# Performance work log

Hardware: AMD Instinct MI355X
Metric: run time of the kernel (lower is better)

The kernel has to match this reference:

```python
import jax, jax.numpy as jnp
import numpy as np

DIM = 1024
DIM_FEAT = 384
HIDDEN = 1024
HEADS = 16
D_HEAD = HIDDEN // HEADS
SCALE = D_HEAD ** -0.5
EPS = 1e-5


def _layernorm(x, g, b):
    mu = jnp.mean(x, axis=-1, keepdims=True)
    var = jnp.var(x, axis=-1, keepdims=True)
    return (x - mu) * jax.lax.rsqrt(var + EPS) * g + b


def _split_heads(t):
    b, n, _ = t.shape
    return t.reshape(b, n, HEADS, D_HEAD).transpose(0, 2, 1, 3)  # b h n d


def _merge_heads(t):
    b, h, n, d = t.shape
    return t.transpose(0, 2, 1, 3).reshape(b, n, h * d)


def _attn(q, k, v):
    dots = jnp.einsum('bhnd,bhmd->bhnm', q, k) * SCALE
    attn = jax.nn.softmax(dots, axis=-1)
    return jnp.einsum('bhnm,bhmd->bhnd', attn, v)


def setup_inputs() -> dict:
    key = jax.random.key(0)
    ks = jax.random.split(key, 10)
    B, N = 2, 2048
    s = lambda fan: 1.0 / np.sqrt(fan)
    return {
        'x': jax.random.normal(ks[0], (B, N, DIM), jnp.float32),
        'feature': jax.random.normal(ks[1], (B, N, DIM_FEAT), jnp.float32),
        'norm_g': jnp.ones((DIM,), jnp.float32),
        'norm_b': jnp.zeros((DIM,), jnp.float32),
        'W_cq': jax.random.normal(ks[2], (DIM, HIDDEN), jnp.float32) * s(DIM),
        'W_ckv': jax.random.normal(ks[3], (DIM_FEAT, 2 * HIDDEN), jnp.float32) * s(DIM_FEAT),
        'W_sqkv': jax.random.normal(ks[4], (DIM, 3 * HIDDEN), jnp.float32) * s(DIM),
        'ffn_g': jnp.ones((DIM,), jnp.float32),
        'ffn_b': jnp.zeros((DIM,), jnp.float32),
        'W1': jax.random.normal(ks[5], (DIM, 4 * DIM), jnp.float32) * s(DIM),
        'b1': jnp.zeros((4 * DIM,), jnp.float32),
        'W2': jax.random.normal(ks[6], (4 * DIM, DIM), jnp.float32) * s(4 * DIM),
        'b2': jnp.zeros((DIM,), jnp.float32),
    }


def reference(x, feature, norm_g, norm_b, W_cq, W_ckv, W_sqkv, ffn_g, ffn_b, W1, b1, W2, b2):
    # cross attention
    xn = _layernorm(x, norm_g, norm_b)
    q = _split_heads(xn @ W_cq)
    kv = feature @ W_ckv
    k, v = jnp.split(kv, 2, axis=-1)
    cross = _merge_heads(_attn(q, _split_heads(k), _split_heads(v))) + x
    # self attention (shared norm)
    cn = _layernorm(cross, norm_g, norm_b)
    qkv = cn @ W_sqkv
    sq, sk, sv = (_split_heads(t) for t in jnp.split(qkv, 3, axis=-1))
    self_tok = _merge_heads(_attn(sq, sk, sv)) + cross
    # FFN with its own layernorm
    h = _layernorm(self_tok, ffn_g, ffn_b)
    h = jax.nn.gelu(h @ W1 + b1, approximate=False)
    out = h @ W2 + b2
    return out + self_tok
```

## Files before the change

kernel.cpp:

```cpp
#include <hip/hip_runtime.h>
#include <math.h>
#include <stdint.h>

typedef __attribute__((ext_vector_type(8)))  short   short8;
typedef __attribute__((ext_vector_type(4)))  short   short4v;
typedef __attribute__((ext_vector_type(8)))  __bf16  bf16x8;
typedef __attribute__((ext_vector_type(4)))  float   f32x4;
typedef __attribute__((ext_vector_type(16))) float   f32x16;

__device__ __forceinline__ unsigned short f2b(float f) {
    union { float f; unsigned u; } v; v.f = f;
    unsigned r = v.u + 0x7FFF + ((v.u >> 16) & 1);
    return (unsigned short)(r >> 16);
}

__device__ __forceinline__ f32x4 mfma_bf16(bf16x8 a, bf16x8 b, f32x4 c) {
    return __builtin_amdgcn_mfma_f32_16x16x32_bf16(a, b, c, 0, 0, 0);
}

__device__ __forceinline__ f32x16 mfma32(bf16x8 a, bf16x8 b, f32x16 c) {
    return __builtin_amdgcn_mfma_f32_32x32x16_bf16(a, b, c, 0, 0, 0);
}

__device__ __forceinline__ unsigned cvt_pk_bf16(float lo, float hi) {
    unsigned r;
    asm volatile("v_cvt_pk_bf16_f32 %0, %1, %2" : "=v"(r) : "v"(lo), "v"(hi));
    return r;
}

__device__ __forceinline__ void gload_lds16(const unsigned short* g, unsigned short* l) {
    __builtin_amdgcn_global_load_lds(
        (const __attribute__((address_space(1))) void*)g,
        (__attribute__((address_space(3))) void*)l,
        16, 0, 0);
}

template <int N>
__device__ __forceinline__ void wait_vmcnt() {
    if constexpr (N == 0)       asm volatile("s_waitcnt vmcnt(0)" ::: "memory");
    else if constexpr (N == 4)  asm volatile("s_waitcnt vmcnt(4)" ::: "memory");
    else if constexpr (N == 6)  asm volatile("s_waitcnt vmcnt(6)" ::: "memory");
    else if constexpr (N == 8)  asm volatile("s_waitcnt vmcnt(8)" ::: "memory");
    else                        static_assert(N == 0 || N == 4 || N == 6 || N == 8, "add vmcnt case");
}

#define QSCALE 0.18033688011112042592f

__global__ __launch_bounds__(256) void wconv_t(const float* __restrict__ W,
                                               unsigned short* __restrict__ Wt,
                                               int K, int N) {
    __shared__ float tile[32][33];
    int bk = blockIdx.x * 32;
    int bn = blockIdx.y * 32;
    int tx = threadIdx.x & 31, ty = threadIdx.x >> 5;
#pragma unroll
    for (int i = 0; i < 4; ++i) {
        int r = ty + i * 8;
        tile[r][tx] = W[(size_t)(bk + r) * N + bn + tx];
    }
    __syncthreads();
#pragma unroll
    for (int i = 0; i < 4; ++i) {
        int r = ty + i * 8;
        Wt[(size_t)(bn + r) * K + bk + tx] = f2b(tile[tx][r]);
    }
}

__global__ __launch_bounds__(256) void fconv(const float* __restrict__ in,
                                             unsigned short* __restrict__ out, int n4) {
    int i = blockIdx.x * 256 + threadIdx.x;
    if (i >= n4) return;
    f32x4 v = ((const f32x4*)in)[i];
    short4v o;
    o.x = (short)f2b(v.x); o.y = (short)f2b(v.y);
    o.z = (short)f2b(v.z); o.w = (short)f2b(v.w);
    ((short4v*)out)[i] = o;
}

__global__ __launch_bounds__(256) void lnorm(const float* __restrict__ x,
                                             const float* __restrict__ g,
                                             const float* __restrict__ bta,
                                             unsigned short* __restrict__ out) {
    int row = blockIdx.x;
    const f32x4* xr = (const f32x4*)(x + (size_t)row * 1024);
    int t = threadIdx.x;
    f32x4 v = xr[t];
    float s  = v.x + v.y + v.z + v.w;
    float s2 = v.x * v.x + v.y * v.y + v.z * v.z + v.w * v.w;
#pragma unroll
    for (int m = 1; m < 64; m <<= 1) {
        s  += __shfl_xor(s, m);
        s2 += __shfl_xor(s2, m);
    }
    __shared__ float rs[8];
    int w = t >> 6;
    if ((t & 63) == 0) { rs[w] = s; rs[4 + w] = s2; }
    __syncthreads();
    s  = rs[0] + rs[1] + rs[2] + rs[3];
    s2 = rs[4] + rs[5] + rs[6] + rs[7];
    float mean = s * (1.0f / 1024.0f);
    float var  = s2 * (1.0f / 1024.0f) - mean * mean;
    float rstd = rsqrtf(var + 1e-5f);
    f32x4 gv = ((const f32x4*)g)[t];
    f32x4 bv = ((const f32x4*)bta)[t];
    short4v o;
    o.x = (short)f2b((v.x - mean) * rstd * gv.x + bv.x);
    o.y = (short)f2b((v.y - mean) * rstd * gv.y + bv.y);
    o.z = (short)f2b((v.z - mean) * rstd * gv.z + bv.z);
    o.w = (short)f2b((v.w - mean) * rstd * gv.w + bv.w);
    ((short4v*)(out + (size_t)row * 1024))[t] = o;
}

template <int WM, int WN, int MI, int NI, int EPI, bool SCQ>
__global__ __launch_bounds__(WM * WN * 64, 2)
void gemm8(const unsigned short* __restrict__ A,
           const unsigned short* __restrict__ Bt,
           void* __restrict__ C,
           const float* __restrict__ bias,
           const float* __restrict__ resid,
           int M, int N, int K, int scale_cols) {
    constexpr int BM = WM * MI * 16;
    constexpr int BN = WN * NI * 16;
    constexpr int THREADS = WM * WN * 64;
    constexpr int ROWS = THREADS / 8;
    constexpr int IA = BM / ROWS;
    constexpr int IB = BN / ROWS;

    const int nwg = gridDim.x;
    const int nby = N / BN;
    int flat = blockIdx.x;
    int wk = (flat & 7) * (nwg >> 3) + (flat >> 3);
    const int m0 = (wk / nby) * BM;
    const int n0 = (wk % nby) * BN;

    __shared__ unsigned short As[2][BM * 64];
    __shared__ unsigned short Bs[2][BN * 64];

    const int tid  = threadIdx.x;
    const int lane = tid & 63;
    const int wid  = tid >> 6;
    const int wm = wid / WN, wn = wid % WN;
    const int l15 = lane & 15, q4 = lane >> 4, xw = lane & 7;

    const int sr = tid >> 3;
    const int sg = (tid & 7) ^ (sr & 7);

    const unsigned short* ag = A  + (size_t)(m0 + sr) * K + sg * 8;
    const unsigned short* bg = Bt + (size_t)(n0 + sr) * K + sg * 8;

    f32x4 acc[MI][NI] = {};

    auto STAGE = [&](int d, int t) {
        const int k0 = t * 64;
#pragma unroll
        for (int i = 0; i < IA; ++i)
            gload_lds16(ag + (size_t)(i * ROWS) * K + k0, &As[d][i * ROWS * 64 + tid * 8]);
#pragma unroll
        for (int i = 0; i < IB; ++i)
            gload_lds16(bg + (size_t)(i * ROWS) * K + k0, &Bs[d][i * ROWS * 64 + tid * 8]);
    };

    const int NT = K >> 6;
    STAGE(0, 0);

    for (int t = 0; t < NT; ++t) {
        const int c = t & 1;
        if (t + 1 < NT) STAGE(c ^ 1, t + 1);
        __builtin_amdgcn_sched_barrier(0);
        if (t + 1 < NT) wait_vmcnt<IA + IB>();
        else            wait_vmcnt<0>();
        __builtin_amdgcn_s_barrier();
        __builtin_amdgcn_sched_barrier(0);
#pragma unroll
        for (int h = 0; h < 2; ++h) {
            bf16x8 a[MI], b[NI];
            const int gsl = h * 4 + q4;
#pragma unroll
            for (int mi = 0; mi < MI; ++mi)
                a[mi] = *(const bf16x8*)&As[c][(wm * MI * 16 + mi * 16 + l15) * 64 + ((gsl ^ xw) << 3)];
#pragma unroll
            for (int ni = 0; ni < NI; ++ni)
                b[ni] = *(const bf16x8*)&Bs[c][(wn * NI * 16 + ni * 16 + l15) * 64 + ((gsl ^ xw) << 3)];
            __builtin_amdgcn_s_setprio(1);
#pragma unroll
            for (int mi = 0; mi < MI; ++mi)
#pragma unroll
                for (int ni = 0; ni < NI; ++ni)
                    acc[mi][ni] = mfma_bf16(a[mi], b[ni], acc[mi][ni]);
            __builtin_amdgcn_s_setprio(0);
        }
        __builtin_amdgcn_sched_barrier(0);
        __builtin_amdgcn_s_barrier();
    }

    const int rb = m0 + wm * MI * 16 + q4 * 4;
    const int cb = n0 + wn * NI * 16 + l15;
    float bv[NI];
    if (EPI >= 1) {
#pragma unroll
        for (int ni = 0; ni < NI; ++ni) bv[ni] = bias[cb + ni * 16];
    }
#pragma unroll
    for (int mi = 0; mi < MI; ++mi) {
#pragma unroll
        for (int r = 0; r < 4; ++r) {
            const int row = rb + mi * 16 + r;
#pragma unroll
            for (int ni = 0; ni < NI; ++ni) {
                const int col = cb + ni * 16;
                float v = acc[mi][ni][r];
                if (EPI == 0) {
                    if (SCQ && col < scale_cols) v *= QSCALE;
                    ((unsigned short*)C)[(size_t)row * N + col] = f2b(v);
                } else if (EPI == 1) {
                    v += bv[ni];
                    v = 0.5f * v * (1.0f + erff(v * 0.70710678118f));
                    ((unsigned short*)C)[(size_t)row * N + col] = f2b(v);
                } else {
                    v += bv[ni] + resid[(size_t)row * N + col];
                    ((float*)C)[(size_t)row * N + col] = v;
                }
            }
        }
    }
}

template <int EPI, bool SCQ>
__global__ __launch_bounds__(512, 2)
void gemm256(const unsigned short* __restrict__ A,
             const unsigned short* __restrict__ Bt,
             void* __restrict__ C,
             const float* __restrict__ bias,
             const float* __restrict__ resid,
             int M, int N, int K, int scale_cols) {
    const int nby = N / 256;
    const int nwg = gridDim.x;
    int flat = blockIdx.x;
    int wk = (flat & 7) * (nwg >> 3) + (flat >> 3);
    const int m0 = (wk / nby) * 256;
    const int n0 = (wk % nby) * 256;

    __shared__ unsigned short As[2][256 * 64];
    __shared__ unsigned short Bs[2][256 * 64];

    const int tid  = threadIdx.x;
    const int lane = tid & 63;
    const int wid  = tid >> 6;
    const int wm = wid >> 2, wn = wid & 3;
    const int l15 = lane & 15, q4 = lane >> 4, xw = lane & 7;

    const int sr = tid >> 3;
    const int sg = (tid & 7) ^ (sr & 7);

    const unsigned short* ag = A  + (size_t)(m0 + sr) * K + sg * 8;
    const unsigned short* bg = Bt + (size_t)(n0 + sr) * K + sg * 8;

    f32x4 acc[8][4] = {};

#define SA256(d, t, i) gload_lds16(ag + (size_t)((i) * 64) * K + (t) * 64, &As[d][(i) * 4096 + tid * 8])
#define SB256(d, t, i) gload_lds16(bg + (size_t)((i) * 64) * K + (t) * 64, &Bs[d][(i) * 4096 + tid * 8])

    const int NT = K >> 6;
#pragma unroll
    for (int i = 0; i < 4; ++i) { SA256(0, 0, i); SB256(0, 0, i); }
    wait_vmcnt<0>();
    __builtin_amdgcn_s_barrier();

    for (int t = 0; t < NT; ++t) {
        const int c = t & 1;
        const bool pf = (t + 1 < NT);
        bf16x8 breg[4];
#pragma unroll
        for (int p = 0; p < 4; ++p) {
            const int h = p >> 1, mh = p & 1;
            const int col = ((h * 4 + q4) ^ xw) << 3;
            if ((p & 1) == 0) {
#pragma unroll
                for (int ni = 0; ni < 4; ++ni)
                    breg[ni] = *(const bf16x8*)&Bs[c][(wn * 64 + ni * 16 + l15) * 64 + col];
            }
            bf16x8 a[4];
#pragma unroll
            for (int mi = 0; mi < 4; ++mi)
                a[mi] = *(const bf16x8*)&As[c][(wm * 128 + mh * 64 + mi * 16 + l15) * 64 + col];
            if (pf) {
                if (p == 0)      { SA256(c ^ 1, t + 1, 0); SB256(c ^ 1, t + 1, 0); SA256(c ^ 1, t + 1, 1); }
                else if (p == 1) { SB256(c ^ 1, t + 1, 1); SA256(c ^ 1, t + 1, 2); SB256(c ^ 1, t + 1, 2); }
                else if (p == 2) { SA256(c ^ 1, t + 1, 3); SB256(c ^ 1, t + 1, 3); }
            }
            __builtin_amdgcn_sched_barrier(0);
            asm volatile("s_waitcnt lgkmcnt(0)" ::: "memory");
            __builtin_amdgcn_sched_barrier(0);
            __builtin_amdgcn_s_setprio(1);
#pragma unroll
            for (int mi = 0; mi < 4; ++mi)
#pragma unroll
                for (int ni = 0; ni < 4; ++ni)
                    acc[mh * 4 + mi][ni] = mfma_bf16(a[mi], breg[ni], acc[mh * 4 + mi][ni]);
            __builtin_amdgcn_s_setprio(0);
            __builtin_amdgcn_sched_barrier(0);
            if (p == 3) wait_vmcnt<0>();
            __builtin_amdgcn_s_barrier();
        }
    }
#undef SA256
#undef SB256

    const int rb = m0 + wm * 128 + q4 * 4;
    const int cb = n0 + wn * 64 + l15;
    float bv[4];
    if (EPI >= 1) {
#pragma unroll
        for (int ni = 0; ni < 4; ++ni) bv[ni] = bias[cb + ni * 16];
    }
#pragma unroll
    for (int ai = 0; ai < 8; ++ai) {
#pragma unroll
        for (int r = 0; r < 4; ++r) {
            const int row = rb + ai * 16 + r;
#pragma unroll
            for (int ni = 0; ni < 4; ++ni) {
                const int col = cb + ni * 16;
                float v = acc[ai][ni][r];
                if (EPI == 0) {
                    if (SCQ && col < scale_cols) v *= QSCALE;
                    ((unsigned short*)C)[(size_t)row * N + col] = f2b(v);
                } else if (EPI == 1) {
                    v += bv[ni];
                    v = 0.5f * v * (1.0f + erff(v * 0.70710678118f));
                    ((unsigned short*)C)[(size_t)row * N + col] = f2b(v);
                } else {
                    v += bv[ni] + resid[(size_t)row * N + col];
                    ((float*)C)[(size_t)row * N + col] = v;
                }
            }
        }
    }
}

__global__ __launch_bounds__(256) void kvpack(const unsigned short* __restrict__ src,
                                              int stride, int k_off, int v_off,
                                              unsigned short* __restrict__ pack) {
    const int oct = blockIdx.x;
    const int bh  = blockIdx.y;
    const int b = bh >> 4, h = bh & 15;
    const int tid = threadIdx.x;
    const int lane = tid & 63;
    const int sl = tid >> 6;
    const int l31 = lane & 31, l5 = lane >> 5;
    __shared__ unsigned short Kl[32 * 64], Vl[32 * 64];
    const int r = tid >> 3, c8 = (tid & 7) * 8;
    for (int t8 = 0; t8 < 8; ++t8) {
        const int kt = oct * 8 + t8;
        const int kb = kt * 32;
        *(short8*)&Kl[r * 64 + c8] = *(const short8*)&src[(size_t)(b * 2048 + kb + r) * stride + k_off + h * 64 + c8];
        *(short8*)&Vl[r * 64 + c8] = *(const short8*)&src[(size_t)(b * 2048 + kb + r) * stride + v_off + h * 64 + c8];
        __syncthreads();
        unsigned short* o = pack + (size_t)bh * 262144 + (size_t)kt * 4096;
        *(short8*)&o[sl * 512 + lane * 8] = *(const short8*)&Kl[l31 * 64 + sl * 16 + l5 * 8];
        {
            const int dh = sl >> 1, c2 = sl & 1;
            short8 vv;
#pragma unroll
            for (int j = 0; j < 8; ++j)
                vv[j] = (short)Vl[(c2 * 16 + l5 * 8 + j) * 64 + dh * 32 + l31];
            *(short8*)&o[(4 + sl) * 512 + lane * 8] = vv;
        }
        __syncthreads();
    }
}

__global__ __launch_bounds__(128) void attn(const unsigned short* __restrict__ Q, int q_stride, int q_off,
                                            const unsigned short* __restrict__ pack,
                                            const float* __restrict__ res,
                                            float* __restrict__ out) {
    const int bid = blockIdx.x;
    const int slot = bid >> 3;
    const int bh = (bid & 7) * 4 + (slot >> 5);
    const int qt = slot & 31;
    const int b = bh >> 4, h = bh & 15;
    const int lane = threadIdx.x & 63, w = threadIdx.x >> 6;
    const int l31 = lane & 31, l5 = lane >> 5;

    __shared__ unsigned short lds[2][8192];

    const int q0 = qt * 64 + w * 32;

    const unsigned short* qp = Q + (size_t)(b * 2048 + q0 + l31) * q_stride + q_off + h * 64 + l5 * 8;
    bf16x8 qf[4];
#pragma unroll
    for (int i = 0; i < 4; ++i) qf[i] = *(const bf16x8*)&qp[i * 16];

    const unsigned short* pkb = pack + (size_t)bh * 262144;

    f32x16 oacc[2] = {};
    f32x16 lacc = {};

    auto STAGE = [&](int d, int t) {
        const unsigned short* s = pkb + (size_t)t * 8192;
#pragma unroll
        for (int i = 0; i < 8; ++i) {
            const int ch = i * 2 + w;
            gload_lds16(s + ch * 512 + lane * 8, &lds[d][ch * 512 + lane * 8]);
        }
    };

    STAGE(0, 0);

    for (int t = 0; t < 32; ++t) {
        const int cur = t & 1;
        if (t + 1 < 32) STAGE(cur ^ 1, t + 1);
        __builtin_amdgcn_sched_barrier(0);
        if (t + 1 < 32) wait_vmcnt<8>();
        else            wait_vmcnt<0>();
        __builtin_amdgcn_s_barrier();
        __builtin_amdgcn_sched_barrier(0);

        const unsigned short* L = &lds[cur][lane * 8];

        bf16x8 kf[2][4];
#pragma unroll
        for (int ks = 0; ks < 2; ++ks)
#pragma unroll
            for (int i = 0; i < 4; ++i)
                kf[ks][i] = *(const bf16x8*)&L[ks * 4096 + i * 512];

        f32x16 s0 = {}, s1 = {};
        __builtin_amdgcn_s_setprio(1);
#pragma unroll
        for (int i = 0; i < 4; ++i) s0 = mfma32(kf[0][i], qf[i], s0);
#pragma unroll
        for (int i = 0; i < 4; ++i) s1 = mfma32(kf[1][i], qf[i], s1);
        __builtin_amdgcn_s_setprio(0);

        bf16x8 vf[2][4];
#pragma unroll
        for (int dh = 0; dh < 2; ++dh)
#pragma unroll
            for (int jj = 0; jj < 4; ++jj)
                vf[dh][jj] = *(const bf16x8*)&L[(jj >> 1) * 4096 + (4 + dh * 2 + (jj & 1)) * 512];

        float p0[16], p1[16];
#pragma unroll
        for (int r = 0; r < 16; ++r) p0[r] = __builtin_amdgcn_exp2f(s0[r]);
#pragma unroll
        for (int r = 0; r < 16; ++r) p1[r] = __builtin_amdgcn_exp2f(s1[r]);
#pragma unroll
        for (int r = 0; r < 16; ++r) lacc[r] += p0[r] + p1[r];

        bf16x8 pf[4];
#pragma unroll
        for (int half = 0; half < 2; ++half) {
            const float* p = half ? p1 : p0;
#pragma unroll
            for (int c = 0; c < 2; ++c) {
                unsigned a0 = cvt_pk_bf16(p[8 * c + 0], p[8 * c + 1]);
                unsigned a1 = cvt_pk_bf16(p[8 * c + 4], p[8 * c + 5]);
                unsigned b0 = cvt_pk_bf16(p[8 * c + 2], p[8 * c + 3]);
                unsigned b1 = cvt_pk_bf16(p[8 * c + 6], p[8 * c + 7]);
                asm volatile("v_permlane32_swap_b32 %0, %1" : "+v"(a0), "+v"(a1));
                asm volatile("v_permlane32_swap_b32 %0, %1" : "+v"(b0), "+v"(b1));
                union { unsigned u[4]; bf16x8 v; } pu;
                pu.u[0] = a0; pu.u[1] = b0; pu.u[2] = a1; pu.u[3] = b1;
                pf[half * 2 + c] = pu.v;
            }
        }

        __builtin_amdgcn_s_setprio(1);
#pragma unroll
        for (int dh = 0; dh < 2; ++dh)
#pragma unroll
            for (int jj = 0; jj < 4; ++jj)
                oacc[dh] = mfma32(vf[dh][jj], pf[jj], oacc[dh]);
        __builtin_amdgcn_s_setprio(0);

        __builtin_amdgcn_s_barrier();
    }

    float lsum[16];
#pragma unroll
    for (int r = 0; r < 16; ++r) lsum[r] = lacc[r];
#pragma unroll
    for (int off = 8; off >= 1; off >>= 1)
#pragma unroll
        for (int r = 0; r < off; ++r) lsum[r] += lsum[r + off];
    const float l = lsum[0] + __shfl_xor(lsum[0], 32);

    const float inv = 1.0f / l;
    const size_t rowoff = (size_t)(b * 2048 + q0 + l31) * 1024 + h * 64;
#pragma unroll
    for (int dh = 0; dh < 2; ++dh) {
#pragma unroll
        for (int g = 0; g < 4; ++g) {
            const int col = dh * 32 + g * 8 + l5 * 4;
            f32x4 rv = *(const f32x4*)&res[rowoff + col];
            f32x4 ov;
#pragma unroll
            for (int r = 0; r < 4; ++r) ov[r] = oacc[dh][g * 4 + r] * inv + rv[r];
            *(f32x4*)&out[rowoff + col] = ov;
        }
    }
}

extern "C" void kernel_launch(void* const* d_in, const int* in_sizes, int n_in,
                              void* d_out, int out_size, void* d_ws, size_t ws_size,
                              hipStream_t stream) {
    const float* x      = (const float*)d_in[0];
    const float* feat   = (const float*)d_in[1];
    const float* norm_g = (const float*)d_in[2];
    const float* norm_b = (const float*)d_in[3];
    const float* W_cq   = (const float*)d_in[4];
    const float* W_ckv  = (const float*)d_in[5];
    const float* W_sqkv = (const float*)d_in[6];
    const float* ffn_g  = (const float*)d_in[7];
    const float* ffn_b  = (const float*)d_in[8];
    const float* W1     = (const float*)d_in[9];
    const float* b1     = (const float*)d_in[10];
    const float* W2     = (const float*)d_in[11];
    const float* b2     = (const float*)d_in[12];
    float* out = (float*)d_out;

    char* ws = (char*)d_ws;
    unsigned short* wq_t   = (unsigned short*)(ws + (size_t)(0u)   * (1u << 20));
    unsigned short* wkv_t  = (unsigned short*)(ws + (size_t)(2u)   * (1u << 20));
    unsigned short* wqkv_t = (unsigned short*)(ws + (size_t)(4u)   * (1u << 20));
    unsigned short* w1_t   = (unsigned short*)(ws + (size_t)(10u)  * (1u << 20));
    unsigned short* w2_t   = (unsigned short*)(ws + (size_t)(18u)  * (1u << 20));
    unsigned short* featb  = (unsigned short*)(ws + (size_t)(26u)  * (1u << 20));
    unsigned short* t0     = (unsigned short*)(ws + (size_t)(29u)  * (1u << 20));
    float*          cross  = (float*)        (ws + (size_t)(37u)  * (1u << 20));
    unsigned short* qb     = (unsigned short*)(ws + (size_t)(53u)  * (1u << 20));
    unsigned short* kvb    = (unsigned short*)(ws + (size_t)(61u)  * (1u << 20));
    unsigned short* qkvb   = (unsigned short*)(ws + (size_t)(77u)  * (1u << 20));
    unsigned short* packb  = (unsigned short*)(ws + (size_t)(101u) * (1u << 20));
    unsigned short* h1     = (unsigned short*)(ws + (size_t)(53u)  * (1u << 20));

    wconv_t<<<dim3(1024 / 32, 1024 / 32), 256, 0, stream>>>(W_cq,   wq_t,   1024, 1024);
    wconv_t<<<dim3(384 / 32,  2048 / 32), 256, 0, stream>>>(W_ckv,  wkv_t,  384,  2048);
    wconv_t<<<dim3(1024 / 32, 3072 / 32), 256, 0, stream>>>(W_sqkv, wqkv_t, 1024, 3072);
    wconv_t<<<dim3(1024 / 32, 4096 / 32), 256, 0, stream>>>(W1,     w1_t,   1024, 4096);
    wconv_t<<<dim3(4096 / 32, 1024 / 32), 256, 0, stream>>>(W2,     w2_t,   4096, 1024);
    fconv<<<dim3((4096 * 384 / 4) / 256), 256, 0, stream>>>(feat, featb, 4096 * 384 / 4);

    lnorm<<<4096, 256, 0, stream>>>(x, norm_g, norm_b, t0);
    gemm8<2, 2, 4, 2, 0, true ><<<512, 256, 0, stream>>>(t0,    wq_t,  qb,  nullptr, nullptr, 4096, 1024, 1024, 1024);
    gemm8<2, 2, 4, 4, 0, false><<<512, 256, 0, stream>>>(featb, wkv_t, kvb, nullptr, nullptr, 4096, 2048, 384,  0);
    kvpack<<<dim3(8, 32), 256, 0, stream>>>(kvb, 2048, 0, 1024, packb);
    attn<<<1024, 128, 0, stream>>>(qb, 1024, 0, packb, x, cross);

    lnorm<<<4096, 256, 0, stream>>>(cross, norm_g, norm_b, t0);
    gemm256<0, true ><<<192, 512, 0, stream>>>(t0, wqkv_t, qkvb, nullptr, nullptr, 4096, 3072, 1024, 1024);
    kvpack<<<dim3(8, 32), 256, 0, stream>>>(qkvb, 3072, 1024, 2048, packb);
    attn<<<1024, 128, 0, stream>>>(qkvb, 3072, 0, packb, cross, out);

    lnorm<<<4096, 256, 0, stream>>>(out, ffn_g, ffn_b, t0);
    gemm256<1, false><<<256, 512, 0, stream>>>(t0, w1_t, h1, b1, nullptr, 4096, 4096, 1024, 0);
    gemm8<2, 2, 4, 2, 2, false><<<512, 256, 0, stream>>>(h1, w2_t, out, b2, (const float*)out, 4096, 1024, 4096, 0);
}
```

Baseline: 332.2 us.

## Split attention key tiles across two waves per query group and merge via LDS

The attention kernel now launches 256 threads per block instead of 128. Each pair of waves shares a 32-query group, and each wave handles one 32-key half of every 64-key tile. The partial output accumulators and row sums are combined through LDS at the end. The aim is more waves per block, and so better latency hiding and MFMA utilisation, at the cost of an LDS reduction, an extra barrier, and redundant Q loads.

```diff
diff --git a/kernel.cpp b/kernel.cpp
--- a/kernel.cpp
+++ b/kernel.cpp
@@ -370,7 +370,7 @@
     }
 }
 
-__global__ __launch_bounds__(128) void attn(const unsigned short* __restrict__ Q, int q_stride, int q_off,
+__global__ __launch_bounds__(256) void attn(const unsigned short* __restrict__ Q, int q_stride, int q_off,
                                             const unsigned short* __restrict__ pack,
                                             const float* __restrict__ res,
                                             float* __restrict__ out) {
@@ -379,12 +379,14 @@
     const int bh = (bid & 7) * 4 + (slot >> 5);
     const int qt = slot & 31;
     const int b = bh >> 4, h = bh & 15;
-    const int lane = threadIdx.x & 63, w = threadIdx.x >> 6;
+    const int tid = threadIdx.x;
+    const int lane = tid & 63, w = tid >> 6;
+    const int qg = w >> 1, ks = w & 1;
     const int l31 = lane & 31, l5 = lane >> 5;
 
     __shared__ unsigned short lds[2][8192];
 
-    const int q0 = qt * 64 + w * 32;
+    const int q0 = qt * 64 + qg * 32;
 
     const unsigned short* qp = Q + (size_t)(b * 2048 + q0 + l31) * q_stride + q_off + h * 64 + l5 * 8;
     bf16x8 qf[4];
@@ -399,8 +401,8 @@
     auto STAGE = [&](int d, int t) {
         const unsigned short* s = pkb + (size_t)t * 8192;
 #pragma unroll
-        for (int i = 0; i < 8; ++i) {
-            const int ch = i * 2 + w;
+        for (int i = 0; i < 4; ++i) {
+            const int ch = i * 4 + w;
             gload_lds16(s + ch * 512 + lane * 8, &lds[d][ch * 512 + lane * 8]);
         }
     };
@@ -411,93 +413,101 @@
         const int cur = t & 1;
         if (t + 1 < 32) STAGE(cur ^ 1, t + 1);
         __builtin_amdgcn_sched_barrier(0);
-        if (t + 1 < 32) wait_vmcnt<8>();
+        if (t + 1 < 32) wait_vmcnt<4>();
         else            wait_vmcnt<0>();
         __builtin_amdgcn_s_barrier();
         __builtin_amdgcn_sched_barrier(0);
 
-        const unsigned short* L = &lds[cur][lane * 8];
-
-        bf16x8 kf[2][4];
-#pragma unroll
-        for (int ks = 0; ks < 2; ++ks)
-#pragma unroll
-            for (int i = 0; i < 4; ++i)
-                kf[ks][i] = *(const bf16x8*)&L[ks * 4096 + i * 512];
-
-        f32x16 s0 = {}, s1 = {};
+        const unsigned short* L = &lds[cur][ks * 4096 + lane * 8];
+
+        bf16x8 kf[4];
+#pragma unroll
+        for (int i = 0; i < 4; ++i) kf[i] = *(const bf16x8*)&L[i * 512];
+
+        f32x16 s = {};
         __builtin_amdgcn_s_setprio(1);
 #pragma unroll
-        for (int i = 0; i < 4; ++i) s0 = mfma32(kf[0][i], qf[i], s0);
-#pragma unroll
-        for (int i = 0; i < 4; ++i) s1 = mfma32(kf[1][i], qf[i], s1);
+        for (int i = 0; i < 4; ++i) s = mfma32(kf[i], qf[i], s);
         __builtin_amdgcn_s_setprio(0);
 
-        bf16x8 vf[2][4];
+        bf16x8 vf[2][2];
 #pragma unroll
         for (int dh = 0; dh < 2; ++dh)
 #pragma unroll
-            for (int jj = 0; jj < 4; ++jj)
-                vf[dh][jj] = *(const bf16x8*)&L[(jj >> 1) * 4096 + (4 + dh * 2 + (jj & 1)) * 512];
-
-        float p0[16], p1[16];
-#pragma unroll
-        for (int r = 0; r < 16; ++r) p0[r] = __builtin_amdgcn_exp2f(s0[r]);
-#pragma unroll
-        for (int r = 0; r < 16; ++r) p1[r] = __builtin_amdgcn_exp2f(s1[r]);
-#pragma unroll
-        for (int r = 0; r < 16; ++r) lacc[r] += p0[r] + p1[r];
-
-        bf16x8 pf[4];
-#pragma unroll
-        for (int half = 0; half < 2; ++half) {
-            const float* p = half ? p1 : p0;
-#pragma unroll
-            for (int c = 0; c < 2; ++c) {
-                unsigned a0 = cvt_pk_bf16(p[8 * c + 0], p[8 * c + 1]);
-                unsigned a1 = cvt_pk_bf16(p[8 * c + 4], p[8 * c + 5]);
-                unsigned b0 = cvt_pk_bf16(p[8 * c + 2], p[8 * c + 3]);
-                unsigned b1 = cvt_pk_bf16(p[8 * c + 6], p[8 * c + 7]);
-                asm volatile("v_permlane32_swap_b32 %0, %1" : "+v"(a0), "+v"(a1));
-                asm volatile("v_permlane32_swap_b32 %0, %1" : "+v"(b0), "+v"(b1));
-                union { unsigned u[4]; bf16x8 v; } pu;
-                pu.u[0] = a0; pu.u[1] = b0; pu.u[2] = a1; pu.u[3] = b1;
-                pf[half * 2 + c] = pu.v;
+            for (int c2 = 0; c2 < 2; ++c2)
+                vf[dh][c2] = *(const bf16x8*)&L[(4 + dh * 2 + c2) * 512];
+
+        float p[16];
+#pragma unroll
+        for (int r = 0; r < 16; ++r) p[r] = __builtin_amdgcn_exp2f(s[r]);
+#pragma unroll
+        for (int r = 0; r < 16; ++r) lacc[r] += p[r];
+
+        bf16x8 pf[2];
+#pragma unroll
+        for (int c = 0; c < 2; ++c) {
+            unsigned a0 = cvt_pk_bf16(p[8 * c + 0], p[8 * c + 1]);
+            unsigned a1 = cvt_pk_bf16(p[8 * c + 4], p[8 * c + 5]);
+            unsigned b0 = cvt_pk_bf16(p[8 * c + 2], p[8 * c + 3]);
+            unsigned b1 = cvt_pk_bf16(p[8 * c + 6], p[8 * c + 7]);
+            asm volatile("v_permlane32_swap_b32 %0, %1" : "+v"(a0), "+v"(a1));
+            asm volatile("v_permlane32_swap_b32 %0, %1" : "+v"(b0), "+v"(b1));
+            union { unsigned u[4]; bf16x8 v; } pu;
+            pu.u[0] = a0; pu.u[1] = b0; pu.u[2] = a1; pu.u[3] = b1;
+            pf[c] = pu.v;
+        }
+
+        __builtin_amdgcn_s_setprio(1);
+#pragma unroll
+        for (int dh = 0; dh < 2; ++dh)
+#pragma unroll
+            for (int c2 = 0; c2 < 2; ++c2)
+                oacc[dh] = mfma32(vf[dh][c2], pf[c2], oacc[dh]);
+        __builtin_amdgcn_s_setprio(0);
+
+        __builtin_amdgcn_s_barrier();
+    }
+
+    float lsum[16];
+#pragma unroll
+    for (int r = 0; r < 16; ++r) lsum[r] = lacc[r];
+#pragma unroll
+    for (int off = 8; off >= 1; off >>= 1)
+#pragma unroll
+        for (int r = 0; r < off; ++r) lsum[r] += lsum[r + off];
+    float lh = lsum[0] + __shfl_xor(lsum[0], 32);
+
+    float* mb = (float*)&lds[qg][0];
+    if (ks == 1) {
+#pragma unroll
+        for (int dh = 0; dh < 2; ++dh)
+#pragma unroll
+            for (int r = 0; r < 16; ++r)
+                mb[lane * 33 + dh * 16 + r] = oacc[dh][r];
+        mb[lane * 33 + 32] = lh;
+    }
+    __syncthreads();
+    if (ks == 0) {
+#pragma unroll
+        for (int dh = 0; dh < 2; ++dh)
+#pragma unroll
+            for (int r = 0; r < 16; ++r)
+                oacc[dh][r] += mb[lane * 33 + dh * 16 + r];
+        const float l = lh + mb[lane * 33 + 32];
+
+        const float inv = 1.0f / l;
+        const size_t rowoff = (size_t)(b * 2048 + q0 + l31) * 1024 + h * 64;
+#pragma unroll
+        for (int dh = 0; dh < 2; ++dh) {
+#pragma unroll
+            for (int g = 0; g < 4; ++g) {
+                const int col = dh * 32 + g * 8 + l5 * 4;
+                f32x4 rv = *(const f32x4*)&res[rowoff + col];
+                f32x4 ov;
+#pragma unroll
+                for (int r = 0; r < 4; ++r) ov[r] = oacc[dh][g * 4 + r] * inv + rv[r];
+                *(f32x4*)&out[rowoff + col] = ov;
             }
-        }
-
-        __builtin_amdgcn_s_setprio(1);
-#pragma unroll
-        for (int dh = 0; dh < 2; ++dh)
-#pragma unroll
-            for (int jj = 0; jj < 4; ++jj)
-                oacc[dh] = mfma32(vf[dh][jj], pf[jj], oacc[dh]);
-        __builtin_amdgcn_s_setprio(0);
-
-        __builtin_amdgcn_s_barrier();
-    }
-
-    float lsum[16];
-#pragma unroll
-    for (int r = 0; r < 16; ++r) lsum[r] = lacc[r];
-#pragma unroll
-    for (int off = 8; off >= 1; off >>= 1)
-#pragma unroll
-        for (int r = 0; r < off; ++r) lsum[r] += lsum[r + off];
-    const float l = lsum[0] + __shfl_xor(lsum[0], 32);
-
-    const float inv = 1.0f / l;
-    const size_t rowoff = (size_t)(b * 2048 + q0 + l31) * 1024 + h * 64;
-#pragma unroll
-    for (int dh = 0; dh < 2; ++dh) {
-#pragma unroll
-        for (int g = 0; g < 4; ++g) {
-            const int col = dh * 32 + g * 8 + l5 * 4;
-            f32x4 rv = *(const f32x4*)&res[rowoff + col];
-            f32x4 ov;
-#pragma unroll
-            for (int r = 0; r < 4; ++r) ov[r] = oacc[dh][g * 4 + r] * inv + rv[r];
-            *(f32x4*)&out[rowoff + col] = ov;
         }
     }
 }
@@ -546,12 +556,12 @@
     gemm8<2, 2, 4, 2, 0, true ><<<512, 256, 0, stream>>>(t0,    wq_t,  qb,  nullptr, nullptr, 4096, 1024, 1024, 1024);
     gemm8<2, 2, 4, 4, 0, false><<<512, 256, 0, stream>>>(featb, wkv_t, kvb, nullptr, nullptr, 4096, 2048, 384,  0);
     kvpack<<<dim3(8, 32), 256, 0, stream>>>(kvb, 2048, 0, 1024, packb);
-    attn<<<1024, 128, 0, stream>>>(qb, 1024, 0, packb, x, cross);
+    attn<<<1024, 256, 0, stream>>>(qb, 1024, 0, packb, x, cross);
 
     lnorm<<<4096, 256, 0, stream>>>(cross, norm_g, norm_b, t0);
     gemm256<0, true ><<<192, 512, 0, stream>>>(t0, wqkv_t, qkvb, nullptr, nullptr, 4096, 3072, 1024, 1024);
     kvpack<<<dim3(8, 32), 256, 0, stream>>>(qkvb, 3072, 1024, 2048, packb);
-    attn<<<1024, 128, 0, stream>>>(qkvb, 3072, 0, packb, cross, out);
+    attn<<<1024, 256, 0, stream>>>(qkvb, 3072, 0, packb, cross, out);
 
     lnorm<<<4096, 256, 0, stream>>>(out, ffn_g, ffn_b, t0);
     gemm256<1, false><<<256, 512, 0, stream>>>(t0, w1_t, h1, b1, nullptr, 4096, 4096, 1024, 0);
```

After: 329.5 us. About the same (-0.8%).
